# Optimization experiments

Hardware: AMD Instinct MI355X
Metric: run time of the kernel (lower is better)

## Reference

```python
import jax, jax.numpy as jnp
import numpy as np

V, D, H, NQ = 32000, 768, 12, 768
B, S = 2, 1024
HD = D // H

def conv1d(x, w, b, pad):
    # x [B,C,L], w [O,I,K]
    y = jax.lax.conv_general_dilated(x, w, (1,), [(pad, pad)], dimension_numbers=('NCH', 'OIH', 'NCH'))
    return y + b[None, :, None]

def maxpool3(x):
    return jax.lax.reduce_window(x, -jnp.inf, jax.lax.max, (1, 1, 3), (1, 1, 1), [(0, 0), (0, 0), (1, 1)])

def ln(x, g, b):
    m = jnp.mean(x, -1, keepdims=True)
    v = jnp.mean((x - m) ** 2, -1, keepdims=True)
    return (x - m) * jax.lax.rsqrt(v + 1e-5) * g + b

def setup_inputs():
    key = jax.random.key(0)
    ks = iter(jax.random.split(key, 64))
    def w(shape, s=0.02):
        return jax.random.normal(next(ks), shape, jnp.float32) * s
    inp = {}
    inp['x'] = jax.random.randint(next(ks), (B, S), 0, V)
    inp['attention_mask'] = jax.random.randint(next(ks), (B, S), 0, 2, dtype=jnp.int32)
    inp['adj_matrix'] = jax.random.uniform(next(ks), (B, S, S), jnp.float32) * (1.0 / S)
    inp['emb'] = w((V, D))
    inp['inc1_w'] = w((64, D, 1)); inp['inc1_b'] = jnp.zeros((64,))
    inp['inc3a_w'] = w((96, D, 1)); inp['inc3a_b'] = jnp.zeros((96,))
    inp['inc3b_w'] = w((128, 96, 3)); inp['inc3b_b'] = jnp.zeros((128,))
    inp['inc5a_w'] = w((16, D, 1)); inp['inc5a_b'] = jnp.zeros((16,))
    inp['inc5b_w'] = w((32, 16, 5)); inp['inc5b_b'] = jnp.zeros((32,))
    inp['incp_w'] = w((32, D, 1)); inp['incp_b'] = jnp.zeros((32,))
    inp['q_rot'] = jax.random.normal(next(ks), (2, NQ, 3), jnp.float32)
    inp['q_ent'] = jax.random.normal(next(ks), (2, NQ - 1), jnp.float32)
    inp['gnn_w1'] = w((D, D // 2)); inp['gnn_b1'] = jnp.zeros((D // 2,))
    inp['gnn_w2'] = w((D // 2, D)); inp['gnn_b2'] = jnp.zeros((D,))
    inp['wq'] = w((D, D)); inp['bq'] = jnp.zeros((D,))
    inp['wk'] = w((D, D)); inp['bk'] = jnp.zeros((D,))
    inp['wv'] = w((D, D)); inp['bv'] = jnp.zeros((D,))
    inp['wo'] = w((D, D)); inp['bo'] = jnp.zeros((D,))
    inp['ff_w1'] = w((D, 4 * D)); inp['ff_b1'] = jnp.zeros((4 * D,))
    inp['ff_w2'] = w((4 * D, D)); inp['ff_b2'] = jnp.zeros((D,))
    inp['ln1_g'] = jnp.ones((D,)); inp['ln1_b'] = jnp.zeros((D,))
    inp['ln2_g'] = jnp.ones((D,)); inp['ln2_b'] = jnp.zeros((D,))
    inp['out_w'] = w((D, V)); inp['out_b'] = jnp.zeros((V,))
    inp['task_w'] = w((D, 3)); inp['task_b'] = jnp.zeros((3,))
    return inp

def reference(x, attention_mask, adj_matrix, emb, inc1_w, inc1_b, inc3a_w, inc3a_b, inc3b_w, inc3b_b, inc5a_w, inc5a_b, inc5b_w, inc5b_b, incp_w, incp_b, q_rot, q_ent, gnn_w1, gnn_b1, gnn_w2, gnn_b2, wq, bq, wk, bk, wv, bv, wo, bo, ff_w1, ff_b1, ff_w2, ff_b2, ln1_g, ln1_b, ln2_g, ln2_b, out_w, out_b, task_w, task_b):
    h = emb[x]                      # [B,S,D]
    hc = h.transpose(0, 2, 1)       # [B,D,S]
    b1 = conv1d(hc, inc1_w, inc1_b, 0)
    b3 = conv1d(conv1d(hc, inc3a_w, inc3a_b, 0), inc3b_w, inc3b_b, 1)
    b5 = conv1d(conv1d(hc, inc5a_w, inc5a_b, 0), inc5b_w, inc5b_b, 2)
    bp = conv1d(maxpool3(hc), incp_w, incp_b, 0)
    h = jnp.concatenate([b1, b3, b5, bp], axis=1).transpose(0, 2, 1)  # [B,S,256]
    # quantum layer: pad 256 -> NQ
    h = jnp.pad(h, ((0, 0), (0, 0), (0, NQ - h.shape[-1])))
    for layer in range(2):
        h = jnp.sin(h[..., None] + q_rot[layer]).sum(-1)          # [B,S,NQ]
        hs = jnp.roll(h, 1, axis=-1)
        h = h[..., :-1] * jnp.sin(q_ent[layer]) + hs[..., :-1] * jnp.cos(q_ent[layer])
        h = jnp.pad(h, ((0, 0), (0, 0), (0, 1)))
    # GNN
    g = jax.nn.relu(jnp.matmul(adj_matrix, h) @ gnn_w1 + gnn_b1)
    h = jnp.matmul(adj_matrix, g) @ gnn_w2 + gnn_b2
    # attention (faithful to original mask-bug: masks where transformed mask == 0)
    am = (1.0 - attention_mask.astype(jnp.float32))[:, None, None, :] * -10000.0
    Q = (h @ wq + bq).reshape(B, S, H, HD).transpose(0, 2, 1, 3)
    K = (h @ wk + bk).reshape(B, S, H, HD).transpose(0, 2, 1, 3)
    Vv = (h @ wv + bv).reshape(B, S, H, HD).transpose(0, 2, 1, 3)
    scores = jnp.einsum('bhqd,bhkd->bhqk', Q, K) / jnp.sqrt(jnp.float32(HD))
    scores = jnp.where(am == 0.0, -1e9, scores)
    attn = jax.nn.softmax(scores, axis=-1)
    ctx = jnp.einsum('bhqk,bhkd->bhqd', attn, Vv).transpose(0, 2, 1, 3).reshape(B, S, D)
    h = ln(h + (ctx @ wo + bo), ln1_g, ln1_b)
    ff = jax.nn.relu(h @ ff_w1 + ff_b1) @ ff_w2 + ff_b2
    h = ln(h + ff, ln2_g, ln2_b)
    token_output = h @ out_w + out_b            # [B,S,V]
    task_output = h.mean(axis=1) @ task_w + task_b  # [B,3]
    return token_output, task_output
```

## Files before the change

### kernel.cpp

```cpp
#include <hip/hip_runtime.h>
#include <hip/hip_bf16.h>

#define B_ 2
#define S_ 1024
#define D_ 768
#define H_ 12
#define HD_ 64
#define V_ 32000
#define NQ_ 768
#define NTOK (B_*S_)
#define QKVS 1572864L

typedef __attribute__((ext_vector_type(8))) short short8;
typedef __attribute__((ext_vector_type(4))) short s16x4;
typedef __attribute__((ext_vector_type(4))) float f32x4;
typedef __attribute__((ext_vector_type(4))) int i32x4;

typedef const __attribute__((address_space(1))) void* as1vp;
typedef __attribute__((address_space(3))) void* as3vp;

__device__ __forceinline__ short f2bf(float f) {
    union { float f; unsigned u; } v; v.f = f;
    unsigned r = (v.u + 0x7FFFu + ((v.u >> 16) & 1u)) >> 16;
    return (short)r;
}
__device__ __forceinline__ float b2fs(short s) {
    union { unsigned u; float f; } v; v.u = ((unsigned)(unsigned short)s) << 16;
    return v.f;
}

__global__ void k_embed2(const int* __restrict__ x, const float* __restrict__ emb,
                         short* __restrict__ h0b, short* __restrict__ mpb) {
    int n = blockIdx.x; int s = n & (S_-1);
    int r0 = x[n];
    int rm = (s > 0)      ? x[n-1] : -1;
    int rp = (s < S_-1)   ? x[n+1] : -1;
    for (int d = threadIdx.x; d < D_; d += blockDim.x) {
        float e = emb[(long)r0*D_ + d];
        float m = e;
        if (rm >= 0) m = fmaxf(m, emb[(long)rm*D_ + d]);
        if (rp >= 0) m = fmaxf(m, emb[(long)rp*D_ + d]);
        h0b[(long)n*D_ + d] = f2bf(e);
        mpb[(long)n*D_ + d] = f2bf(m);
    }
}

__global__ __launch_bounds__(256) void k_mix(
    const float* __restrict__ CO, const float* __restrict__ c3w,
    const float* __restrict__ c3b, const float* __restrict__ c5w,
    const float* __restrict__ c5b, const float* __restrict__ q_rot,
    const float* __restrict__ q_ent, float* __restrict__ h1f)
{
    __shared__ float co[5][176];
    __shared__ float ta[NQ_];
    __shared__ float tb[NQ_];
    int n = blockIdx.x; int s = n & (S_-1);
    int t = threadIdx.x;
    for (int idx = t; idx < 5*176; idx += 256) {
        int dr = idx / 176 - 2, c = idx % 176;
        int ss = s + dr;
        co[idx/176][c] = (ss >= 0 && ss < S_) ? CO[(long)(n + dr)*176 + c] : 0.f;
    }
    for (int d = 256 + t; d < NQ_; d += 256) ta[d] = 0.f;
    __syncthreads();
    if (t < 64) {
        ta[t] = co[2][t];
    } else if (t < 192) {
        int o = t - 64;
        float acc = c3b[o];
        #pragma unroll
        for (int k = 0; k < 3; k++)
            for (int i = 0; i < 96; i++)
                acc += co[1+k][64+i] * c3w[(o*96+i)*3 + k];
        ta[t] = acc;
    } else if (t < 224) {
        int o = t - 192;
        float acc = c5b[o];
        #pragma unroll
        for (int k = 0; k < 5; k++)
            for (int i = 0; i < 16; i++)
                acc += co[k][160+i] * c5w[(o*16+i)*5 + k];
        ta[t] = acc;
    } else {
        ta[t] = h1f[(long)n*NQ_ + t];
    }
    __syncthreads();
    #pragma unroll
    for (int layer = 0; layer < 2; layer++) {
        const float* rot = q_rot + (long)layer*NQ_*3;
        const float* ent = q_ent + (long)layer*(NQ_-1);
        for (int q = t; q < NQ_; q += 256) {
            float hv = ta[q];
            tb[q] = __sinf(hv + rot[q*3]) + __sinf(hv + rot[q*3+1]) + __sinf(hv + rot[q*3+2]);
        }
        __syncthreads();
        for (int q = t; q < NQ_; q += 256) {
            float v;
            if (q == NQ_-1) v = 0.f;
            else {
                int qm = (q == 0) ? (NQ_-1) : (q-1);
                v = tb[q]*__sinf(ent[q]) + tb[qm]*__cosf(ent[q]);
            }
            ta[q] = v;
        }
        __syncthreads();
    }
    for (int q = t; q < NQ_; q += 256) h1f[(long)n*NQ_ + q] = ta[q];
}

template<int AMODE, int OMODE, bool RELU, int KSPLIT = 1>
__global__ __launch_bounds__(256) void k_bgemm(
    const short* __restrict__ A, const short* __restrict__ Bm,
    void* __restrict__ Cv, float* __restrict__ C2,
    const float* __restrict__ bias, float scale,
    int N, int K, int lda, int ldb, int ldc,
    long sA, long sB, long sC)
{
    __shared__ short lds[2][8192];
    const int t = threadIdx.x;
    const int lane = t & 63, wave = t >> 6;
    const int wm = wave >> 1, wn = wave & 1;
    const int l15 = lane & 15, l4 = lane >> 4;

    int bx = blockIdx.x, by = blockIdx.y;
    if (KSPLIT == 1 && gridDim.z == 1) {
        int lin = by * gridDim.x + bx;
        int nwg = gridDim.x * gridDim.y;
        int xcd = lin & 7, pos = lin >> 3;
        int q = nwg >> 3, r = nwg & 7;
        int lin2 = (xcd < r ? xcd*(q+1) : r*(q+1) + (xcd-r)*q) + pos;
        bx = lin2 % gridDim.x;
        by = lin2 / gridDim.x;
    }
    const int tile_m = bx * 128, tile_n = by * 128;
    const int kz = (KSPLIT > 1) ? blockIdx.z : 0;
    const int Keff = K / KSPLIT;
    const int kbase = kz * Keff;
    const long aoff = (KSPLIT > 1) ? 0 : (long)blockIdx.z * sA;
    const long boff = (KSPLIT > 1) ? 0 : (long)blockIdx.z * sB;
    const long coff = (KSPLIT > 1) ? 0 : (long)blockIdx.z * sC;

    const int cA0 = t, cA1 = t + 256;
    const int arow0 = tile_m + ((cA0 >> 6) << 4) + (cA0 & 15);
    const int arow1 = tile_m + ((cA1 >> 6) << 4) + (cA1 & 15);
    const int akb0 = ((cA0 >> 4) & 3) * 8;
    const int akb1 = ((cA1 >> 4) & 3) * 8;
    const int bcol0 = tile_n + (((cA0 >> 4) & 7) << 4) + (cA0 & 15);
    const int bcol1 = tile_n + (((cA1 >> 4) & 7) << 4) + (cA1 & 15);
    const int bkb0 = (cA0 >> 7) * 8;
    const int bkb1 = (cA1 >> 7) * 8;
    const short* bp0 = Bm + boff + (long)bcol0*ldb + bkb0 + kbase;
    const short* bp1 = Bm + boff + (long)bcol1*ldb + bkb1 + kbase;
    const short* ap0 = nullptr; const short* ap1 = nullptr;
    long abase0 = 0, abase1 = 0;
    if (AMODE == 0) {
        ap0 = A + aoff + (long)arow0*lda + akb0 + kbase;
        ap1 = A + aoff + (long)arow1*lda + akb1 + kbase;
    } else {
        abase0 = ((long)((arow0 >> 10)*H_) * S_ + (arow0 & (S_-1))) * 64;
        abase1 = ((long)((arow1 >> 10)*H_) * S_ + (arow1 & (S_-1))) * 64;
    }
    const int wb = wave * 1024;

    auto stage = [&](int buf, int k0) {
        char* lb = (char*)&lds[buf][0];
        const short *a0, *a1;
        if (AMODE == 0) { a0 = ap0 + k0; a1 = ap1 + k0; }
        else {
            int ka0 = kbase + k0 + akb0, ka1 = kbase + k0 + akb1;
            a0 = A + abase0 + (long)(ka0 >> 6)*(S_*64) + (ka0 & 63);
            a1 = A + abase1 + (long)(ka1 >> 6)*(S_*64) + (ka1 & 63);
        }
        __builtin_amdgcn_global_load_lds((as1vp)a0,          (as3vp)(lb + wb),          16, 0, 0);
        __builtin_amdgcn_global_load_lds((as1vp)a1,          (as3vp)(lb + 4096 + wb),   16, 0, 0);
        __builtin_amdgcn_global_load_lds((as1vp)(bp0 + k0),  (as3vp)(lb + 8192 + wb),   16, 0, 0);
        __builtin_amdgcn_global_load_lds((as1vp)(bp1 + k0),  (as3vp)(lb + 12288 + wb),  16, 0, 0);
    };

    f32x4 acc[4][4] = {};
    const int nk = Keff >> 5;
    stage(0, 0);
    __syncthreads();
    int cur = 0;
    for (int ks = 0; ks < nk; ks++) {
        if (ks + 1 < nk) stage(cur ^ 1, (ks + 1) << 5);
        short8 af[4], bfv[4];
        const short* lb = &lds[cur][0];
        #pragma unroll
        for (int m = 0; m < 4; m++)
            af[m] = *(const short8*)(lb + (wm*4 + m)*512 + l4*128 + l15*8);
        #pragma unroll
        for (int n = 0; n < 4; n++)
            bfv[n] = *(const short8*)(lb + 4096 + l4*1024 + (wn*4 + n)*128 + l15*8);
        #pragma unroll
        for (int m = 0; m < 4; m++)
            #pragma unroll
            for (int n = 0; n < 4; n++)
                acc[m][n] = __builtin_amdgcn_mfma_f32_16x16x32_bf16(af[m], bfv[n], acc[m][n], 0, 0, 0);
        __syncthreads();
        cur ^= 1;
    }

    #pragma unroll
    for (int m = 0; m < 4; m++) {
        #pragma unroll
        for (int n = 0; n < 4; n++) {
            int col = tile_n + wn*64 + n*16 + l15;
            if (col >= N) continue;
            float bv = (bias && (KSPLIT == 1 || kz == 0)) ? bias[col] : 0.f;
            #pragma unroll
            for (int r = 0; r < 4; r++) {
                int row = tile_m + wm*64 + m*16 + l4*4 + r;
                float v = acc[m][n][r] * scale + bv;
                if (RELU) v = fmaxf(v, 0.f);
                if (OMODE == 0) {
                    if (KSPLIT > 1)
                        atomicAdd(&((float*)Cv)[(long)row*ldc + col], v);
                    else
                        ((float*)Cv)[coff + (long)row*ldc + col] = v;
                } else if (OMODE == 1) {
                    ((short*)Cv)[coff + (long)row*ldc + col] = f2bf(v);
                } else if (OMODE == 2) {
                    C2[coff + (long)row*ldc + col] = v;
                    ((short*)Cv)[coff + (long)row*ldc + col] = f2bf(v);
                } else {
                    int seg = (col >= 1536) ? 2 : ((col >= 768) ? 1 : 0);
                    int c = col - seg*768;
                    int hh = c >> 6, dd = c & 63;
                    int b = row >> 10, s = row & (S_-1);
                    long hidx = (long)(b*H_ + hh);
                    short* base = (short*)Cv;
                    if (seg < 2) base[(long)seg*QKVS + (hidx*S_ + s)*64 + dd] = f2bf(v);
                    else         base[2L*QKVS + (hidx*64 + dd)*S_ + s] = f2bf(v);
                }
            }
        }
    }
}

__global__ __launch_bounds__(512, 1) void k_vgemm(
    const short* __restrict__ A, const short* __restrict__ Bm,
    float* __restrict__ C, const float* __restrict__ bias,
    int N, int K, int lda, int ldb, int ldc)
{
    extern __shared__ short lds[];
    const int t = threadIdx.x;
    const int lane = t & 63, wave = t >> 6;
    const int wm = wave >> 2, wn = wave & 3;
    const int l15 = lane & 15, l4 = lane >> 4;
    int bx = blockIdx.x, by = blockIdx.y;
    {
        int lin = by * gridDim.x + bx;
        int nwg = gridDim.x * gridDim.y;
        int xcd = lin & 7, pos = lin >> 3;
        int q = nwg >> 3, r = nwg & 7;
        int lin2 = (xcd < r ? xcd*(q+1) : r*(q+1) + (xcd-r)*q) + pos;
        bx = lin2 % gridDim.x; by = lin2 / gridDim.x;
    }
    const int tile_m = bx * 256, tile_n = by * 256;

    const int c0 = wave*128 + lane;
    const int c1 = c0 + 64;
    const int ar0 = ((c0 >> 6) << 4) + (c0 & 15), ak0 = ((c0 >> 4) & 3) << 3;
    const int ar1 = ((c1 >> 6) << 4) + (c1 & 15), ak1 = ((c1 >> 4) & 3) << 3;
    const short* pa0 = A + (long)(tile_m + ar0)*lda + ak0;
    const short* pa1 = A + (long)(tile_m + ar1)*lda + ak1;
    const short* pb0 = Bm + (long)(tile_n + ar0)*ldb + ak0;
    const short* pb1 = Bm + (long)(tile_n + ar1)*ldb + ak1;
    char* lb = (char*)lds;
    const int wb0 = wave*2048, wb1 = wave*2048 + 1024;

    auto stage = [&](int reg, int s) {
        int k = s << 5;
        char* ab = lb + reg*32768;
        __builtin_amdgcn_global_load_lds((as1vp)(pa0 + k), (as3vp)(ab + wb0),         16, 0, 0);
        __builtin_amdgcn_global_load_lds((as1vp)(pa1 + k), (as3vp)(ab + wb1),         16, 0, 0);
        __builtin_amdgcn_global_load_lds((as1vp)(pb0 + k), (as3vp)(ab + 16384 + wb0), 16, 0, 0);
        __builtin_amdgcn_global_load_lds((as1vp)(pb1 + k), (as3vp)(ab + 16384 + wb1), 16, 0, 0);
    };

    f32x4 acc[8][4] = {};
    const int nks = K >> 5;
    stage(0, 0); stage(1, 1); stage(2, 2);
    const int ard = ((wm*8) << 10) + (l4 << 8) + l15*16;
    const int brd = 16384 + ((wn*4) << 10) + (l4 << 8) + l15*16;

    int reg = 0;
    for (int s = 0; s < nks; s++) {
        if (s + 3 < nks) {
            int r3 = reg + 3; if (r3 >= 5) r3 -= 5;
            stage(r3, s + 3);
        }
        if (s < nks - 3)       asm volatile("s_waitcnt vmcnt(12)" ::: "memory");
        else if (s == nks - 3) asm volatile("s_waitcnt vmcnt(8)"  ::: "memory");
        else if (s == nks - 2) asm volatile("s_waitcnt vmcnt(4)"  ::: "memory");
        else                   asm volatile("s_waitcnt vmcnt(0)"  ::: "memory");
        __builtin_amdgcn_s_barrier();
        const char* rb = lb + reg*32768;
        short8 a[8], b[4];
        #pragma unroll
        for (int fr = 0; fr < 8; fr++) a[fr] = *(const short8*)(rb + ard + (fr << 10));
        #pragma unroll
        for (int fc = 0; fc < 4; fc++) b[fc] = *(const short8*)(rb + brd + (fc << 10));
        __builtin_amdgcn_s_setprio(1);
        #pragma unroll
        for (int fr = 0; fr < 8; fr++)
            #pragma unroll
            for (int fc = 0; fc < 4; fc++)
                acc[fr][fc] = __builtin_amdgcn_mfma_f32_16x16x32_bf16(a[fr], b[fc], acc[fr][fc], 0, 0, 0);
        __builtin_amdgcn_s_setprio(0);
        if (++reg == 5) reg = 0;
    }

    #pragma unroll
    for (int fr = 0; fr < 8; fr++) {
        #pragma unroll
        for (int fc = 0; fc < 4; fc++) {
            int col = tile_n + wn*64 + fc*16 + l15;
            float bv = bias ? bias[col] : 0.f;
            #pragma unroll
            for (int rr = 0; rr < 4; rr++) {
                int row = tile_m + wm*128 + fr*16 + l4*4 + rr;
                C[(long)row*ldc + col] = acc[fr][fc][rr] + bv;
            }
        }
    }
}

__global__ void k_f2b(const float* __restrict__ in, short* __restrict__ out, long n) {
    long i = ((long)blockIdx.x*256 + threadIdx.x)*4;
    if (i >= n) return;
    f32x4 v = *(const f32x4*)(in + i);
    out[i+0] = f2bf(v.x); out[i+1] = f2bf(v.y); out[i+2] = f2bf(v.z); out[i+3] = f2bf(v.w);
}

struct PrepArgs {
    const float *w1, *w3, *w5, *wp;
    const float *b1, *b3, *b5, *bq, *bk, *bv;
    short *wincat, *wincp;
    float *binc, *bqkv;
};
__global__ void k_prep(PrepArgs a) {
    int blk = blockIdx.x, t = threadIdx.x;
    const float* src; short* dst; long base;
    if (blk < 48)       { src = a.w1; dst = a.wincat;          base = (long)blk*1024; }
    else if (blk < 120) { src = a.w3; dst = a.wincat + 49152;  base = (long)(blk-48)*1024; }
    else if (blk < 132) { src = a.w5; dst = a.wincat + 122880; base = (long)(blk-120)*1024; }
    else if (blk < 156) { src = a.wp; dst = a.wincp;           base = (long)(blk-132)*1024; }
    else {
        if (t < 176) a.binc[t] = (t < 64) ? a.b1[t] : (t < 160 ? a.b3[t-64] : a.b5[t-160]);
        for (int i = t; i < 2304; i += 256)
            a.bqkv[i] = (i < 768) ? a.bq[i] : (i < 1536 ? a.bk[i-768] : a.bv[i-1536]);
        return;
    }
    long i = base + (long)t*4;
    f32x4 v = *(const f32x4*)(src + i);
    dst[i+0] = f2bf(v.x); dst[i+1] = f2bf(v.y); dst[i+2] = f2bf(v.z); dst[i+3] = f2bf(v.w);
}

template<bool RELU>
__global__ void k_t2b(const float* __restrict__ in, short* __restrict__ out,
                      int R, int C, long sIn, long sOut) {
    __shared__ float tile[32][33];
    int bc = blockIdx.x * 32, br = blockIdx.y * 32;
    const float* ip = in + (long)blockIdx.z * sIn;
    short* op = out + (long)blockIdx.z * sOut;
    int tx = threadIdx.x & 31, ty = threadIdx.x >> 5;
    #pragma unroll
    for (int i = 0; i < 32; i += 8)
        tile[ty + i][tx] = ip[(long)(br + ty + i)*C + bc + tx];
    __syncthreads();
    #pragma unroll
    for (int i = 0; i < 32; i += 8) {
        float v = tile[tx][ty + i];
        if (RELU) v = fmaxf(v, 0.f);
        op[(long)(bc + ty + i)*R + br + tx] = f2bf(v);
    }
}

struct T4Args { const float *s0, *s1, *s2, *s3; short* dst; };
__global__ void k_t2b4(T4Args a) {
    __shared__ float tile[32][33];
    int z = blockIdx.z;
    const float* ip = (z == 0) ? a.s0 : (z == 1) ? a.s1 : (z == 2) ? a.s2 : a.s3;
    short* op = a.dst + (long)z * 589824;
    int bc = blockIdx.x * 32, br = blockIdx.y * 32;
    int tx = threadIdx.x & 31, ty = threadIdx.x >> 5;
    #pragma unroll
    for (int i = 0; i < 32; i += 8)
        tile[ty + i][tx] = ip[(long)(br + ty + i)*D_ + bc + tx];
    __syncthreads();
    #pragma unroll
    for (int i = 0; i < 32; i += 8)
        op[(long)(bc + ty + i)*D_ + br + tx] = f2bf(tile[tx][ty + i]);
}

__global__ __launch_bounds__(256) void k_softmax(const short* __restrict__ sc,
                                                 short* __restrict__ P,
                                                 const int* __restrict__ mask) {
    __shared__ float red[256];
    long row = blockIdx.x;
    int b = (int)(row >> 10) / H_;
    const short* r = sc + row * S_;
    short* pr = P + row * S_;
    const int* mrow = mask + b * S_;
    int t = threadIdx.x;
    s16x4 sv = *(const s16x4*)(r + 4*t);
    i32x4 mv = *(const i32x4*)(mrow + 4*t);
    float v[4]; float mx = -1e30f;
    #pragma unroll
    for (int j = 0; j < 4; j++) {
        float s = b2fs(sv[j]);
        if (mv[j] == 1) s = -1e9f;
        v[j] = s; mx = fmaxf(mx, s);
    }
    red[t] = mx; __syncthreads();
    for (int off = 128; off > 0; off >>= 1) {
        if (t < off) red[t] = fmaxf(red[t], red[t+off]);
        __syncthreads();
    }
    mx = red[0]; __syncthreads();
    float sum = 0.f;
    #pragma unroll
    for (int j = 0; j < 4; j++) { v[j] = expf(v[j] - mx); sum += v[j]; }
    red[t] = sum; __syncthreads();
    for (int off = 128; off > 0; off >>= 1) {
        if (t < off) red[t] += red[t+off];
        __syncthreads();
    }
    float inv = 1.f / red[0];
    s16x4 pv;
    #pragma unroll
    for (int j = 0; j < 4; j++) pv[j] = f2bf(v[j] * inv);
    *(s16x4*)(pr + 4*t) = pv;
}

__global__ void k_addln(const float* __restrict__ a, const float* __restrict__ bvec,
                        const float* __restrict__ g, const float* __restrict__ be,
                        float* __restrict__ outf, short* __restrict__ outb) {
    __shared__ float row[D_];
    __shared__ float red[256];
    int n = blockIdx.x, t = threadIdx.x;
    float lsum = 0.f;
    for (int d = t; d < D_; d += 256) {
        float v = a[(long)n*D_ + d] + bvec[(long)n*D_ + d];
        row[d] = v; lsum += v;
    }
    red[t] = lsum; __syncthreads();
    for (int off = 128; off > 0; off >>= 1) {
        if (t < off) red[t] += red[t+off];
        __syncthreads();
    }
    float mean = red[0] / D_; __syncthreads();
    float lvar = 0.f;
    for (int d = t; d < D_; d += 256) { float v = row[d]-mean; lvar += v*v; }
    red[t] = lvar; __syncthreads();
    for (int off = 128; off > 0; off >>= 1) {
        if (t < off) red[t] += red[t+off];
        __syncthreads();
    }
    float rstd = rsqrtf(red[0]/D_ + 1e-5f);
    for (int d = t; d < D_; d += 256) {
        float v = (row[d]-mean)*rstd*g[d] + be[d];
        if (outf) outf[(long)n*D_ + d] = v;
        outb[(long)n*D_ + d] = f2bf(v);
    }
}

__global__ __launch_bounds__(256) void k_pool(const short* __restrict__ h,
                                              float* __restrict__ pooled) {
    int blk = blockIdx.x;
    int b = blk >> 4, ch = blk & 15;
    int t = threadIdx.x;
    float s0 = 0.f, s1 = 0.f, s2 = 0.f;
    for (int ss = ch*64; ss < ch*64 + 64; ss++) {
        const short* row = h + (long)(b*S_ + ss)*D_;
        s0 += b2fs(row[t]);
        s1 += b2fs(row[t + 256]);
        s2 += b2fs(row[t + 512]);
    }
    atomicAdd(&pooled[b*D_ + t],       s0 * (1.f/S_));
    atomicAdd(&pooled[b*D_ + t + 256], s1 * (1.f/S_));
    atomicAdd(&pooled[b*D_ + t + 512], s2 * (1.f/S_));
}

__global__ __launch_bounds__(256) void k_task(const float* __restrict__ pooled,
                                              const float* __restrict__ tw,
                                              const float* __restrict__ tb,
                                              float* __restrict__ out) {
    __shared__ float red[256][3];
    int b = blockIdx.x, t = threadIdx.x;
    float a0 = 0.f, a1 = 0.f, a2 = 0.f;
    for (int d = t; d < D_; d += 256) {
        float p = pooled[b*D_ + d];
        a0 += p*tw[d*3+0]; a1 += p*tw[d*3+1]; a2 += p*tw[d*3+2];
    }
    red[t][0] = a0; red[t][1] = a1; red[t][2] = a2;
    __syncthreads();
    for (int off = 128; off > 0; off >>= 1) {
        if (t < off) {
            red[t][0] += red[t+off][0];
            red[t][1] += red[t+off][1];
            red[t][2] += red[t+off][2];
        }
        __syncthreads();
    }
    if (t < 3) out[(long)NTOK*V_ + b*3 + t] = red[0][t] + tb[t];
}

extern "C" void kernel_launch(void* const* d_in, const int* in_sizes, int n_in,
                              void* d_out, int out_size, void* d_ws, size_t ws_size,
                              hipStream_t stream) {
    const int*   x      = (const int*)d_in[0];
    const int*   amask  = (const int*)d_in[1];
    const float* adj    = (const float*)d_in[2];
    const float* emb    = (const float*)d_in[3];
    const float* inc1_w = (const float*)d_in[4];  const float* inc1_b = (const float*)d_in[5];
    const float* inc3a_w= (const float*)d_in[6];  const float* inc3a_b= (const float*)d_in[7];
    const float* inc3b_w= (const float*)d_in[8];  const float* inc3b_b= (const float*)d_in[9];
    const float* inc5a_w= (const float*)d_in[10]; const float* inc5a_b= (const float*)d_in[11];
    const float* inc5b_w= (const float*)d_in[12]; const float* inc5b_b= (const float*)d_in[13];
    const float* incp_w = (const float*)d_in[14]; const float* incp_b = (const float*)d_in[15];
    const float* q_rot  = (const float*)d_in[16]; const float* q_ent  = (const float*)d_in[17];
    const float* gnn_w1 = (const float*)d_in[18]; const float* gnn_b1 = (const float*)d_in[19];
    const float* gnn_w2 = (const float*)d_in[20]; const float* gnn_b2 = (const float*)d_in[21];
    const float* wq = (const float*)d_in[22]; const float* bq = (const float*)d_in[23];
    const float* wk = (const float*)d_in[24]; const float* bk = (const float*)d_in[25];
    const float* wv = (const float*)d_in[26]; const float* bv = (const float*)d_in[27];
    const float* wo = (const float*)d_in[28]; const float* bo = (const float*)d_in[29];
    const float* ff_w1 = (const float*)d_in[30]; const float* ff_b1 = (const float*)d_in[31];
    const float* ff_w2 = (const float*)d_in[32]; const float* ff_b2 = (const float*)d_in[33];
    const float* ln1_g = (const float*)d_in[34]; const float* ln1_b = (const float*)d_in[35];
    const float* ln2_g = (const float*)d_in[36]; const float* ln2_b = (const float*)d_in[37];
    const float* out_w = (const float*)d_in[38]; const float* out_b = (const float*)d_in[39];
    const float* task_w= (const float*)d_in[40]; const float* task_b= (const float*)d_in[41];

    float* F = (float*)d_out;
    short* wqkvt = (short*)(F + 0L);
    short* gw1t  = (short*)(F + 1179648L);
    short* gw2t  = (short*)(F + 1327104L);
    short* fw1t  = (short*)(F + 1474560L);
    short* fw2t  = (short*)(F + 2654208L);
    short* wincat= (short*)(F + 3833856L);
    short* wincp = (short*)(F + 3950592L);
    float* binc  = F + 4012032L;
    float* bqkv  = F + 4012288L;
    short* adjb  = (short*)(F + 4014592L);
    short* h0b   = (short*)(F + 5063168L);
    short* mpb   = (short*)(F + 5849600L);
    float* CO    = F + 6636032L;
    float* h1f   = F + 6996480L;
    short* h1t   = (short*)(F + 8569344L);
    short* t1b   = (short*)(F + 9355776L);
    float* gbf   = F + 10142208L;
    short* gt    = (short*)(F + 10928640L);
    short* t2bv  = (short*)(F + 11321856L);
    float* h2f   = F + 11715072L;
    short* h2b   = (short*)(F + 13287936L);
    short* Qh    = (short*)(F + 14074368L);
    short* Kh    = (short*)(F + 14860800L);
    short* Vt    = (short*)(F + 15647232L);
    short* ctxh  = (short*)(F + 16499200L);
    float* ao    = F + 17285632L;
    float* hlnf  = F + 18858496L;
    short* hlnb  = (short*)(F + 20431360L);
    short* ff1b  = (short*)(F + 21217792L);
    float* ao2   = F + 24363520L;
    short* scob  = (short*)(F + 25936384L);
    short* Pb    = (short*)(F + 51102208L);

    char* W = (char*)d_ws;
    short* hfb    = (short*)(W + 0);
    float* pooled = (float*)(W + 3145728);
    short* owt    = (short*)(W + 3151872);

    auto gb = [](int M, int N, int Z) { return dim3((unsigned)(M/128), (unsigned)((N+127)/128), (unsigned)Z); };

    hipFuncSetAttribute((const void*)k_vgemm, hipFuncAttributeMaxDynamicSharedMemorySize, 163840);

    hipMemsetAsync(gbf, 0, (size_t)NTOK*384*4, stream);
    hipMemsetAsync(ao,  0, (size_t)NTOK*D_*4, stream);
    hipMemsetAsync(ao2, 0, (size_t)NTOK*D_*4, stream);
    hipMemsetAsync(CO,  0, (size_t)NTOK*176*4, stream);
    hipMemsetAsync(h1f, 0, (size_t)NTOK*NQ_*4, stream);
    hipMemsetAsync(pooled, 0, (size_t)B_*D_*4, stream);

    {
        T4Args t4{wq, wk, wv, wo, wqkvt};
        k_t2b4<<<dim3(24,24,4), 256, 0, stream>>>(t4);
    }
    k_t2b<false><<<dim3(12,24,1), 256, 0, stream>>>(gnn_w1, gw1t, D_, 384, 0, 0);
    k_t2b<false><<<dim3(24,12,1), 256, 0, stream>>>(gnn_w2, gw2t, 384, D_, 0, 0);
    k_t2b<false><<<dim3(96,24,1), 256, 0, stream>>>(ff_w1, fw1t, D_, 4*D_, 0, 0);
    k_t2b<false><<<dim3(24,96,1), 256, 0, stream>>>(ff_w2, fw2t, 4*D_, D_, 0, 0);
    k_t2b<false><<<dim3(1000,24,1), 256, 0, stream>>>(out_w, owt, D_, V_, 0, 0);
    k_f2b<<<dim3(2048), 256, 0, stream>>>(adj, adjb, (long)B_*S_*S_);
    {
        PrepArgs pa{inc1_w, inc3a_w, inc5a_w, incp_w,
                    inc1_b, inc3a_b, inc5a_b, bq, bk, bv,
                    wincat, wincp, binc, bqkv};
        k_prep<<<dim3(157), 256, 0, stream>>>(pa);
    }

    k_embed2<<<dim3(NTOK), dim3(256), 0, stream>>>(x, emb, h0b, mpb);

    k_bgemm<0,0,false,4><<<gb(NTOK, 176, 4), 256, 0, stream>>>(
        h0b, wincat, CO, nullptr, binc, 1.f, 176, D_, D_, D_, 176, 0, 0, 0);
    k_bgemm<0,0,false,8><<<gb(NTOK, 32, 8), 256, 0, stream>>>(
        mpb, wincp, h1f + 224, nullptr, incp_b, 1.f, 32, D_, D_, D_, NQ_, 0, 0, 0);

    k_mix<<<dim3(NTOK), dim3(256), 0, stream>>>(
        CO, inc3b_w, inc3b_b, inc5b_w, inc5b_b, q_rot, q_ent, h1f);

    k_t2b<false><<<dim3(24,32,2), 256, 0, stream>>>(h1f, h1t, S_, NQ_, (long)S_*NQ_, (long)S_*NQ_);
    k_bgemm<0,1,false><<<gb(S_, NQ_, B_), 256, 0, stream>>>(
        adjb, h1t, t1b, nullptr, nullptr, 1.f, NQ_, S_, S_, S_, NQ_,
        (long)S_*S_, (long)NQ_*S_, (long)S_*NQ_);
    k_bgemm<0,0,false,4><<<gb(NTOK, 384, 4), 256, 0, stream>>>(
        t1b, gw1t, gbf, nullptr, gnn_b1, 1.f, 384, D_, D_, D_, 384, 0, 0, 0);
    k_t2b<true><<<dim3(12,32,2), 256, 0, stream>>>(gbf, gt, S_, 384, (long)S_*384, (long)S_*384);
    k_bgemm<0,1,false><<<gb(S_, 384, B_), 256, 0, stream>>>(
        adjb, gt, t2bv, nullptr, nullptr, 1.f, 384, S_, S_, S_, 384,
        (long)S_*S_, (long)384*S_, (long)S_*384);
    k_bgemm<0,2,false><<<gb(NTOK, D_, 1), 256, 0, stream>>>(
        t2bv, gw2t, h2b, h2f, gnn_b2, 1.f, D_, 384, 384, 384, D_, 0, 0, 0);

    k_bgemm<0,5,false><<<gb(NTOK, 3*D_, 1), 256, 0, stream>>>(
        h2b, wqkvt, Qh, nullptr, bqkv, 1.f, 3*D_, D_, D_, D_, 0, 0, 0, 0);
    k_bgemm<0,1,false><<<gb(S_, S_, B_*H_), 256, 0, stream>>>(
        Qh, Kh, scob, nullptr, nullptr, 0.125f, S_, HD_, HD_, HD_, S_,
        (long)S_*HD_, (long)S_*HD_, (long)S_*S_);
    k_softmax<<<dim3(B_*H_*S_), 256, 0, stream>>>(scob, Pb, amask);
    k_bgemm<0,1,false><<<gb(S_, HD_, B_*H_), 256, 0, stream>>>(
        Pb, Vt, ctxh, nullptr, nullptr, 1.f, HD_, S_, S_, S_, HD_,
        (long)S_*S_, (long)HD_*S_, (long)S_*HD_);
    k_bgemm<1,0,false,2><<<gb(NTOK, D_, 2), 256, 0, stream>>>(
        ctxh, wqkvt + 3L*589824, ao, nullptr, bo, 1.f, D_, D_, D_, D_, D_, 0, 0, 0);
    k_addln<<<dim3(NTOK), dim3(256), 0, stream>>>(h2f, ao, ln1_g, ln1_b, hlnf, hlnb);

    k_bgemm<0,1,true><<<gb(NTOK, 4*D_, 1), 256, 0, stream>>>(
        hlnb, fw1t, ff1b, nullptr, ff_b1, 1.f, 4*D_, D_, D_, D_, 4*D_, 0, 0, 0);
    k_bgemm<0,0,false,4><<<gb(NTOK, D_, 4), 256, 0, stream>>>(
        ff1b, fw2t, ao2, nullptr, ff_b2, 1.f, D_, 4*D_, 4*D_, 4*D_, D_, 0, 0, 0);
    k_addln<<<dim3(NTOK), dim3(256), 0, stream>>>(hlnf, ao2, ln2_g, ln2_b, nullptr, hfb);

    k_pool<<<dim3(B_*16), dim3(256), 0, stream>>>(hfb, pooled);
    k_vgemm<<<dim3(NTOK/256, V_/256, 1), dim3(512), 163840, stream>>>(
        hfb, owt, (float*)d_out, out_b, V_, D_, D_, D_, V_);
    k_task<<<dim3(B_), dim3(256), 0, stream>>>(pooled, task_w, task_b, (float*)d_out);
}
```

Before: 703.5 us.

## Fuse attention into flash-style kernel and merge weight prep launches

Replaces the separate QK^T GEMM, softmax kernel and PV GEMM with a single online-softmax attention kernel that keeps scores in registers and stages probabilities through LDS per wave. This removes writing and reading the B*H*S*S bf16 score and probability matrices to global memory. Also merges the many transpose and bf16 conversion launches for weights and adj into one large kernel to cut launch overhead. The fused kernel reads K and V straight from global with no LDS reuse across waves, and uses fast exp, which may shift numerics slightly.

```diff
diff --git a/kernel.cpp b/kernel.cpp
--- a/kernel.cpp
+++ b/kernel.cpp
@@ -327,35 +327,156 @@
     }
 }
 
-__global__ void k_f2b(const float* __restrict__ in, short* __restrict__ out, long n) {
-    long i = ((long)blockIdx.x*256 + threadIdx.x)*4;
-    if (i >= n) return;
-    f32x4 v = *(const f32x4*)(in + i);
-    out[i+0] = f2bf(v.x); out[i+1] = f2bf(v.y); out[i+2] = f2bf(v.z); out[i+3] = f2bf(v.w);
-}
-
-struct PrepArgs {
-    const float *w1, *w3, *w5, *wp;
-    const float *b1, *b3, *b5, *bq, *bk, *bv;
-    short *wincat, *wincp;
+__global__ __launch_bounds__(256) void k_fattn(
+    const short* __restrict__ Q, const short* __restrict__ K,
+    const short* __restrict__ Vt, const int* __restrict__ mask,
+    short* __restrict__ ctx)
+{
+    __shared__ short plds[4096];
+    const int t = threadIdx.x;
+    const int lane = t & 63, wave = t >> 6;
+    const int l15 = lane & 15, l4 = lane >> 4;
+    const int qt = blockIdx.x, z = blockIdx.y;
+    const int b = z / H_;
+    const long zb = (long)z * S_ * 64;
+
+    const int q = qt*64 + wave*16 + l15;
+    short8 aq0 = *(const short8*)(Q + zb + (long)q*64 + l4*8);
+    short8 aq1 = *(const short8*)(Q + zb + (long)q*64 + l4*8 + 32);
+
+    float m[4] = {-1e30f, -1e30f, -1e30f, -1e30f};
+    float l[4] = {0.f, 0.f, 0.f, 0.f};
+    f32x4 O[4] = {};
+    short* pw = plds + wave*1024;
+
+    for (int kt = 0; kt < 16; kt++) {
+        const int kvb = kt*64;
+        f32x4 s[4] = {};
+        #pragma unroll
+        for (int ct = 0; ct < 4; ct++) {
+            const short* kp = K + zb + (long)(kvb + ct*16 + l15)*64 + l4*8;
+            short8 b0 = *(const short8*)(kp);
+            short8 b1 = *(const short8*)(kp + 32);
+            s[ct] = __builtin_amdgcn_mfma_f32_16x16x32_bf16(aq0, b0, s[ct], 0, 0, 0);
+            s[ct] = __builtin_amdgcn_mfma_f32_16x16x32_bf16(aq1, b1, s[ct], 0, 0, 0);
+        }
+        float p[4][4];
+        float rmax[4] = {-1e30f, -1e30f, -1e30f, -1e30f};
+        #pragma unroll
+        for (int ct = 0; ct < 4; ct++) {
+            int mv = mask[b*S_ + kvb + ct*16 + l15];
+            #pragma unroll
+            for (int r = 0; r < 4; r++) {
+                float v = (mv == 1) ? -1e9f : s[ct][r]*0.125f;
+                p[ct][r] = v;
+                rmax[r] = fmaxf(rmax[r], v);
+            }
+        }
+        #pragma unroll
+        for (int r = 0; r < 4; r++) {
+            float v = rmax[r];
+            v = fmaxf(v, __shfl_xor(v, 1));
+            v = fmaxf(v, __shfl_xor(v, 2));
+            v = fmaxf(v, __shfl_xor(v, 4));
+            v = fmaxf(v, __shfl_xor(v, 8));
+            float mn = fmaxf(m[r], v);
+            float corr = __expf(m[r] - mn);
+            float srow = 0.f;
+            #pragma unroll
+            for (int ct = 0; ct < 4; ct++) {
+                float e = __expf(p[ct][r] - mn);
+                p[ct][r] = e;
+                srow += e;
+            }
+            srow += __shfl_xor(srow, 1);
+            srow += __shfl_xor(srow, 2);
+            srow += __shfl_xor(srow, 4);
+            srow += __shfl_xor(srow, 8);
+            l[r] = l[r]*corr + srow;
+            m[r] = mn;
+            #pragma unroll
+            for (int c2 = 0; c2 < 4; c2++) O[c2][r] *= corr;
+        }
+        #pragma unroll
+        for (int ct = 0; ct < 4; ct++)
+            #pragma unroll
+            for (int r = 0; r < 4; r++)
+                pw[(l4*4 + r)*64 + ct*16 + l15] = f2bf(p[ct][r]);
+        asm volatile("s_waitcnt lgkmcnt(0)" ::: "memory");
+        __builtin_amdgcn_sched_barrier(0);
+        short8 pa0 = *(const short8*)(pw + l15*64 + l4*8);
+        short8 pa1 = *(const short8*)(pw + l15*64 + l4*8 + 32);
+        #pragma unroll
+        for (int c2 = 0; c2 < 4; c2++) {
+            const short* vp = Vt + zb + (long)(c2*16 + l15)*S_ + kvb + l4*8;
+            short8 v0 = *(const short8*)(vp);
+            short8 v1 = *(const short8*)(vp + 32);
+            O[c2] = __builtin_amdgcn_mfma_f32_16x16x32_bf16(pa0, v0, O[c2], 0, 0, 0);
+            O[c2] = __builtin_amdgcn_mfma_f32_16x16x32_bf16(pa1, v1, O[c2], 0, 0, 0);
+        }
+    }
+    #pragma unroll
+    for (int r = 0; r < 4; r++) {
+        float inv = 1.f / l[r];
+        int qo = qt*64 + wave*16 + l4*4 + r;
+        #pragma unroll
+        for (int c2 = 0; c2 < 4; c2++)
+            ctx[zb + (long)qo*64 + c2*16 + l15] = f2bf(O[c2][r] * inv);
+    }
+}
+
+struct WPArgs {
+    const float *ow, *wq, *wk, *wv, *wo, *g1, *g2, *f1, *f2, *adj;
+    const float *w1, *w3, *w5, *wp, *b1, *b3, *b5, *bq, *bk, *bv;
+    short *owt, *wqkvt, *gw1t, *gw2t, *fw1t, *fw2t, *adjb, *wincat, *wincp;
     float *binc, *bqkv;
 };
-__global__ void k_prep(PrepArgs a) {
+__global__ __launch_bounds__(256) void k_wprep(WPArgs a) {
+    __shared__ float tile[32][33];
     int blk = blockIdx.x, t = threadIdx.x;
-    const float* src; short* dst; long base;
-    if (blk < 48)       { src = a.w1; dst = a.wincat;          base = (long)blk*1024; }
-    else if (blk < 120) { src = a.w3; dst = a.wincat + 49152;  base = (long)(blk-48)*1024; }
-    else if (blk < 132) { src = a.w5; dst = a.wincat + 122880; base = (long)(blk-120)*1024; }
-    else if (blk < 156) { src = a.wp; dst = a.wincp;           base = (long)(blk-132)*1024; }
-    else {
-        if (t < 176) a.binc[t] = (t < 64) ? a.b1[t] : (t < 160 ? a.b3[t-64] : a.b5[t-160]);
-        for (int i = t; i < 2304; i += 256)
-            a.bqkv[i] = (i < 768) ? a.bq[i] : (i < 1536 ? a.bk[i-768] : a.bv[i-1536]);
+    const float* src; short* dst;
+    int R, C, bx, by;
+    if (blk < 24000)      { src = a.ow; dst = a.owt; R = 768; C = 32000; bx = blk % 1000; by = blk / 1000; }
+    else if (blk < 26304) { int r = blk - 24000; int z = r / 576; r %= 576;
+        src = (z == 0) ? a.wq : (z == 1) ? a.wk : (z == 2) ? a.wv : a.wo;
+        dst = a.wqkvt + (long)z*589824; R = 768; C = 768; bx = r % 24; by = r / 24; }
+    else if (blk < 26592) { int r = blk - 26304; src = a.g1; dst = a.gw1t; R = 768; C = 384;  bx = r % 12; by = r / 12; }
+    else if (blk < 26880) { int r = blk - 26592; src = a.g2; dst = a.gw2t; R = 384; C = 768;  bx = r % 24; by = r / 24; }
+    else if (blk < 29184) { int r = blk - 26880; src = a.f1; dst = a.fw1t; R = 768; C = 3072; bx = r % 96; by = r / 96; }
+    else if (blk < 31488) { int r = blk - 29184; src = a.f2; dst = a.fw2t; R = 3072; C = 768; bx = r % 24; by = r / 24; }
+    else if (blk < 33536) {
+        long i = ((long)(blk - 31488)*256 + t)*4;
+        f32x4 v = *(const f32x4*)(a.adj + i);
+        a.adjb[i+0] = f2bf(v.x); a.adjb[i+1] = f2bf(v.y);
+        a.adjb[i+2] = f2bf(v.z); a.adjb[i+3] = f2bf(v.w);
         return;
-    }
-    long i = base + (long)t*4;
-    f32x4 v = *(const f32x4*)(src + i);
-    dst[i+0] = f2bf(v.x); dst[i+1] = f2bf(v.y); dst[i+2] = f2bf(v.z); dst[i+3] = f2bf(v.w);
+    } else {
+        int r = blk - 33536;
+        const float* s2; short* d2; long base;
+        if (r < 48)       { s2 = a.w1; d2 = a.wincat;          base = (long)r*1024; }
+        else if (r < 120) { s2 = a.w3; d2 = a.wincat + 49152;  base = (long)(r-48)*1024; }
+        else if (r < 132) { s2 = a.w5; d2 = a.wincat + 122880; base = (long)(r-120)*1024; }
+        else if (r < 156) { s2 = a.wp; d2 = a.wincp;           base = (long)(r-132)*1024; }
+        else {
+            if (t < 176) a.binc[t] = (t < 64) ? a.b1[t] : (t < 160 ? a.b3[t-64] : a.b5[t-160]);
+            for (int i = t; i < 2304; i += 256)
+                a.bqkv[i] = (i < 768) ? a.bq[i] : (i < 1536 ? a.bk[i-768] : a.bv[i-1536]);
+            return;
+        }
+        long i = base + (long)t*4;
+        f32x4 v = *(const f32x4*)(s2 + i);
+        d2[i+0] = f2bf(v.x); d2[i+1] = f2bf(v.y); d2[i+2] = f2bf(v.z); d2[i+3] = f2bf(v.w);
+        return;
+    }
+    int bc = bx*32, br = by*32;
+    int tx = t & 31, ty = t >> 5;
+    #pragma unroll
+    for (int i = 0; i < 32; i += 8)
+        tile[ty + i][tx] = src[(long)(br + ty + i)*C + bc + tx];
+    __syncthreads();
+    #pragma unroll
+    for (int i = 0; i < 32; i += 8)
+        dst[(long)(bc + ty + i)*R + br + tx] = f2bf(tile[tx][ty + i]);
 }
 
 template<bool RELU>
@@ -376,63 +497,6 @@
         if (RELU) v = fmaxf(v, 0.f);
         op[(long)(bc + ty + i)*R + br + tx] = f2bf(v);
     }
-}
-
-struct T4Args { const float *s0, *s1, *s2, *s3; short* dst; };
-__global__ void k_t2b4(T4Args a) {
-    __shared__ float tile[32][33];
-    int z = blockIdx.z;
-    const float* ip = (z == 0) ? a.s0 : (z == 1) ? a.s1 : (z == 2) ? a.s2 : a.s3;
-    short* op = a.dst + (long)z * 589824;
-    int bc = blockIdx.x * 32, br = blockIdx.y * 32;
-    int tx = threadIdx.x & 31, ty = threadIdx.x >> 5;
-    #pragma unroll
-    for (int i = 0; i < 32; i += 8)
-        tile[ty + i][tx] = ip[(long)(br + ty + i)*D_ + bc + tx];
-    __syncthreads();
-    #pragma unroll
-    for (int i = 0; i < 32; i += 8)
-        op[(long)(bc + ty + i)*D_ + br + tx] = f2bf(tile[tx][ty + i]);
-}
-
-__global__ __launch_bounds__(256) void k_softmax(const short* __restrict__ sc,
-                                                 short* __restrict__ P,
-                                                 const int* __restrict__ mask) {
-    __shared__ float red[256];
-    long row = blockIdx.x;
-    int b = (int)(row >> 10) / H_;
-    const short* r = sc + row * S_;
-    short* pr = P + row * S_;
-    const int* mrow = mask + b * S_;
-    int t = threadIdx.x;
-    s16x4 sv = *(const s16x4*)(r + 4*t);
-    i32x4 mv = *(const i32x4*)(mrow + 4*t);
-    float v[4]; float mx = -1e30f;
-    #pragma unroll
-    for (int j = 0; j < 4; j++) {
-        float s = b2fs(sv[j]);
-        if (mv[j] == 1) s = -1e9f;
-        v[j] = s; mx = fmaxf(mx, s);
-    }
-    red[t] = mx; __syncthreads();
-    for (int off = 128; off > 0; off >>= 1) {
-        if (t < off) red[t] = fmaxf(red[t], red[t+off]);
-        __syncthreads();
-    }
-    mx = red[0]; __syncthreads();
-    float sum = 0.f;
-    #pragma unroll
-    for (int j = 0; j < 4; j++) { v[j] = expf(v[j] - mx); sum += v[j]; }
-    red[t] = sum; __syncthreads();
-    for (int off = 128; off > 0; off >>= 1) {
-        if (t < off) red[t] += red[t+off];
-        __syncthreads();
-    }
-    float inv = 1.f / red[0];
-    s16x4 pv;
-    #pragma unroll
-    for (int j = 0; j < 4; j++) pv[j] = f2bf(v[j] * inv);
-    *(s16x4*)(pr + 4*t) = pv;
 }
 
 __global__ void k_addln(const float* __restrict__ a, const float* __restrict__ bvec,
@@ -566,8 +630,6 @@
     short* hlnb  = (short*)(F + 20431360L);
     short* ff1b  = (short*)(F + 21217792L);
     float* ao2   = F + 24363520L;
-    short* scob  = (short*)(F + 25936384L);
-    short* Pb    = (short*)(F + 51102208L);
 
     char* W = (char*)d_ws;
     short* hfb    = (short*)(W + 0);
@@ -586,20 +648,16 @@
     hipMemsetAsync(pooled, 0, (size_t)B_*D_*4, stream);
 
     {
-        T4Args t4{wq, wk, wv, wo, wqkvt};
-        k_t2b4<<<dim3(24,24,4), 256, 0, stream>>>(t4);
-    }
-    k_t2b<false><<<dim3(12,24,1), 256, 0, stream>>>(gnn_w1, gw1t, D_, 384, 0, 0);
-    k_t2b<false><<<dim3(24,12,1), 256, 0, stream>>>(gnn_w2, gw2t, 384, D_, 0, 0);
-    k_t2b<false><<<dim3(96,24,1), 256, 0, stream>>>(ff_w1, fw1t, D_, 4*D_, 0, 0);
-    k_t2b<false><<<dim3(24,96,1), 256, 0, stream>>>(ff_w2, fw2t, 4*D_, D_, 0, 0);
-    k_t2b<false><<<dim3(1000,24,1), 256, 0, stream>>>(out_w, owt, D_, V_, 0, 0);
-    k_f2b<<<dim3(2048), 256, 0, stream>>>(adj, adjb, (long)B_*S_*S_);
-    {
-        PrepArgs pa{inc1_w, inc3a_w, inc5a_w, incp_w,
-                    inc1_b, inc3a_b, inc5a_b, bq, bk, bv,
-                    wincat, wincp, binc, bqkv};
-        k_prep<<<dim3(157), 256, 0, stream>>>(pa);
+        WPArgs wa;
+        wa.ow = out_w; wa.wq = wq; wa.wk = wk; wa.wv = wv; wa.wo = wo;
+        wa.g1 = gnn_w1; wa.g2 = gnn_w2; wa.f1 = ff_w1; wa.f2 = ff_w2; wa.adj = adj;
+        wa.w1 = inc1_w; wa.w3 = inc3a_w; wa.w5 = inc5a_w; wa.wp = incp_w;
+        wa.b1 = inc1_b; wa.b3 = inc3a_b; wa.b5 = inc5a_b;
+        wa.bq = bq; wa.bk = bk; wa.bv = bv;
+        wa.owt = owt; wa.wqkvt = wqkvt; wa.gw1t = gw1t; wa.gw2t = gw2t;
+        wa.fw1t = fw1t; wa.fw2t = fw2t; wa.adjb = adjb;
+        wa.wincat = wincat; wa.wincp = wincp; wa.binc = binc; wa.bqkv = bqkv;
+        k_wprep<<<dim3(33693), 256, 0, stream>>>(wa);
     }
 
     k_embed2<<<dim3(NTOK), dim3(256), 0, stream>>>(x, emb, h0b, mpb);
@@ -627,13 +685,7 @@
 
     k_bgemm<0,5,false><<<gb(NTOK, 3*D_, 1), 256, 0, stream>>>(
         h2b, wqkvt, Qh, nullptr, bqkv, 1.f, 3*D_, D_, D_, D_, 0, 0, 0, 0);
-    k_bgemm<0,1,false><<<gb(S_, S_, B_*H_), 256, 0, stream>>>(
-        Qh, Kh, scob, nullptr, nullptr, 0.125f, S_, HD_, HD_, HD_, S_,
-        (long)S_*HD_, (long)S_*HD_, (long)S_*S_);
-    k_softmax<<<dim3(B_*H_*S_), 256, 0, stream>>>(scob, Pb, amask);
-    k_bgemm<0,1,false><<<gb(S_, HD_, B_*H_), 256, 0, stream>>>(
-        Pb, Vt, ctxh, nullptr, nullptr, 1.f, HD_, S_, S_, S_, HD_,
-        (long)S_*S_, (long)HD_*S_, (long)S_*HD_);
+    k_fattn<<<dim3(S_/64, B_*H_), 256, 0, stream>>>(Qh, Kh, Vt, amask, ctxh);
     k_bgemm<1,0,false,2><<<gb(NTOK, D_, 2), 256, 0, stream>>>(
         ctxh, wqkvt + 3L*589824, ao, nullptr, bo, 1.f, D_, D_, D_, D_, D_, 0, 0, 0);
     k_addln<<<dim3(NTOK), dim3(256), 0, stream>>>(h2f, ao, ln1_g, ln1_b, hlnf, hlnb);
```

Result: faster. 640.2 us (-9.0%).
